# Performance work log

Measured on AMD Instinct MI355X. Metric: run time of the kernel, lower is better.

Reference implementation:

```python
import jax, jax.numpy as jnp
import numpy as np
from jax import lax

VOCAB = 50257; IN_DIM = 1024; MEM = 1024
ATT_UNITS = 256; HOPS = 16
H1 = 1024; H2 = 512; H3 = 256; CLASSES = 5
N = 512  # maxlen == number of tree nodes (pad() is a no-op, penalty mask is zero)


def _build_tree(n):
    # Binary heap tree relabeled to DFS post-order ranks, so children always
    # have smaller rank than their parent and H accumulates in the same order
    # as the original recursive torch code.
    order = []
    def post(j):
        for c in (2 * j + 1, 2 * j + 2):
            if c < n:
                post(c)
        order.append(j)
    post(0)
    rank = {j: r for r, j in enumerate(order)}
    child_idx = np.zeros((n, 2), np.int32)
    mask = np.zeros((n, 2), np.float32)
    for j in range(n):
        r = rank[j]
        for k, c in enumerate((2 * j + 1, 2 * j + 2)):
            if c < n:
                child_idx[r, k] = rank[c]
                mask[r, k] = 1.0
    return jnp.asarray(child_idx), jnp.asarray(mask)


def setup_inputs() -> dict:
    key = jax.random.key(0)
    ks = jax.random.split(key, 24)
    def w(k, shape, s=0.05):
        return jax.random.normal(k, shape, jnp.float32) * s
    child_idx, child_mask = _build_tree(N)
    return {
        "linputs": jax.random.randint(ks[0], (N,), 0, VOCAB, jnp.int32),
        "rinputs": jax.random.randint(ks[1], (N,), 0, VOCAB, jnp.int32),
        "child_idx": child_idx,
        "child_mask": child_mask,
        "emb": w(ks[2], (VOCAB, IN_DIM)),
        "w_ioux": w(ks[3], (3 * MEM, IN_DIM)), "b_ioux": w(ks[4], (3 * MEM,)),
        "w_iouh": w(ks[5], (3 * MEM, MEM)), "b_iouh": w(ks[6], (3 * MEM,)),
        "w_fx": w(ks[7], (MEM, IN_DIM)), "b_fx": w(ks[8], (MEM,)),
        "w_fh": w(ks[9], (MEM, MEM)), "b_fh": w(ks[10], (MEM,)),
        "ws1": w(ks[11], (ATT_UNITS, MEM)),
        "ws2": w(ks[12], (HOPS, ATT_UNITS)),
        "wf": w(ks[13], (1, MEM, H1)),
        "w_lat": w(ks[14], (1, HOPS)), "b_lat": w(ks[15], (1,)),
        "w_fc": w(ks[16], (H2, 3 * H1)), "b_fc": w(ks[17], (H2,)),
        "w_out": w(ks[18], (H3, H2)), "b_out": w(ks[19], (H3,)),
        "w_out1": w(ks[20], (CLASSES, H3)), "b_out1": w(ks[21], (CLASSES,)),
    }


def _tree_lstm(x, child_idx, child_mask, w_ioux, b_ioux, w_iouh, b_iouh,
               w_fx, b_fx, w_fh, b_fh):
    # x: [N, in_dim]; nodes in post-order (children before parent).
    # Leaf case of the original (single all-zero child) is reproduced exactly
    # by masked (zero) child rows: child_h_sum = 0 and sum(f * child_c) = 0.
    n = x.shape[0]
    mem = w_fh.shape[0]
    x_iou = x @ w_ioux.T + b_ioux  # [N, 3M], precomputed input projections
    x_f = x @ w_fx.T + b_fx        # [N, M]

    def step(carry, xs):
        C, Hs = carry
        i, ci, m, xiou, xf = xs
        ch = Hs[ci] * m[:, None]   # [2, M] masked child hidden states
        cc = C[ci] * m[:, None]    # [2, M] masked child cell states
        iou = xiou + ch.sum(0) @ w_iouh.T + b_iouh
        ig, og, ug = jnp.split(iou, 3)
        ig = jax.nn.sigmoid(ig); og = jax.nn.sigmoid(og); ug = jnp.tanh(ug)
        f = jax.nn.sigmoid(ch @ w_fh.T + b_fh + xf)  # [2, M] forget per child
        c = ig * ug + (f * cc).sum(0)
        h = og * jnp.tanh(c)
        return (C.at[i].set(c), Hs.at[i].set(h)), None

    z = jnp.zeros((n, mem), x.dtype)
    (C, Hs), _ = lax.scan(step, (z, z),
                          (jnp.arange(n), child_idx, child_mask, x_iou, x_f))
    return Hs  # H stacked in DFS post-order; root hidden is Hs[-1]


def _attend(H, ws1, ws2):
    # H: [N, M]; N == maxlen so the penalty term of the original is all-zero.
    hbar = jnp.tanh(H @ ws1.T)                           # [N, att_units]
    alphas = jax.nn.softmax((hbar @ ws2.T).T, axis=-1)   # [hops, N]
    return alphas @ H, alphas[None]                      # [hops, M], [1, hops, N]


def reference(linputs, rinputs, child_idx, child_mask, emb,
              w_ioux, b_ioux, w_iouh, b_iouh, w_fx, b_fx, w_fh, b_fh,
              ws1, ws2, wf, w_lat, b_lat, w_fc, b_fc, w_out, b_out,
              w_out1, b_out1):
    tl = lambda tok: _tree_lstm(emb[tok], child_idx, child_mask,
                                w_ioux, b_ioux, w_iouh, b_iouh,
                                w_fx, b_fx, w_fh, b_fh)
    Hl = tl(linputs)
    Hr = tl(rinputs)
    Ml, attl = _attend(Hl, ws1, ws2)
    Mr, attr = _attend(Hr, ws1, ws2)
    lstate = jax.nn.relu(Ml @ wf[0])   # [hops, H1]
    rstate = jax.nn.relu(Mr @ wf[0])
    # lat_att applied on transposed matrix == left-multiply by its weight row
    lvec = w_lat @ lstate + b_lat      # [1, H1]
    rvec = w_lat @ rstate + b_lat
    fr = jnp.concatenate([jnp.abs(lvec - rvec), lvec * rvec,
                          0.5 * (lvec + rvec)], axis=1)  # [1, 3*H1]
    fc = jax.nn.leaky_relu(fr @ w_fc.T + b_fc, 0.01)
    fc2 = jax.nn.sigmoid(fc @ w_out.T + b_out)
    out = jax.nn.log_softmax(fc2 @ w_out1.T + b_out1, axis=-1)  # [1, classes]
    return out, attl, attr
```

## Files before the change

### kernel.cpp

```cpp
#include <hip/hip_runtime.h>
#include <math.h>

#define NN 512
#define MEMD 1024
#define NBLK 256

typedef __attribute__((ext_vector_type(8))) short short8;
typedef __attribute__((ext_vector_type(4))) float float4v;

struct Sched {
  int child0[NN]; int child1[NN];
  float m0[NN]; float m1[NN];
  int chrow[2 * NN];
  int order[NN];
  int lvl_off[12];
};

constexpr void post_order_rec(int j, int n, int (&ord)[NN], int& cnt) {
  if (2 * j + 1 < n) post_order_rec(2 * j + 1, n, ord, cnt);
  if (2 * j + 2 < n) post_order_rec(2 * j + 2, n, ord, cnt);
  ord[cnt++] = j;
}

constexpr Sched make_sched() {
  Sched s{};
  int ord[NN] = {}; int cnt = 0;
  post_order_rec(0, NN, ord, cnt);
  int rank[NN] = {};
  for (int r = 0; r < NN; ++r) rank[ord[r]] = r;
  for (int j = 0; j < NN; ++j) {
    int r = rank[j];
    int c0 = 2 * j + 1, c1 = 2 * j + 2;
    s.child0[r] = (c0 < NN) ? rank[c0] : 0;
    s.m0[r] = (c0 < NN) ? 1.0f : 0.0f;
    s.child1[r] = (c1 < NN) ? rank[c1] : 0;
    s.m1[r] = (c1 < NN) ? 1.0f : 0.0f;
  }
  int h[NN] = {};
  for (int r = 0; r < NN; ++r) {
    int hh = 0;
    if (s.m0[r] > 0.0f) { int t = h[s.child0[r]] + 1; if (t > hh) hh = t; }
    if (s.m1[r] > 0.0f) { int t = h[s.child1[r]] + 1; if (t > hh) hh = t; }
    h[r] = hh;
  }
  int counts[12] = {};
  for (int r = 0; r < NN; ++r) counts[h[r]]++;
  s.lvl_off[0] = 0;
  for (int l = 0; l < 11; ++l) s.lvl_off[l + 1] = s.lvl_off[l] + counts[l];
  int pos[12] = {};
  for (int l = 0; l < 12; ++l) pos[l] = s.lvl_off[l];
  for (int r = 0; r < NN; ++r) s.order[pos[h[r]]++] = r;
  for (int slot = 0; slot < NN; ++slot) {
    int r = s.order[slot];
    s.chrow[2 * slot + 0] = (s.m0[r] > 0.f) ? s.child0[r] : -1;
    s.chrow[2 * slot + 1] = (s.m1[r] > 0.f) ? s.child1[r] : -1;
  }
  return s;
}

static constexpr Sched g_sched = make_sched();
__constant__ Sched c_sched = g_sched;

__device__ __forceinline__ float sigm(float x) { return 1.0f / (1.0f + expf(-x)); }

__device__ __forceinline__ unsigned short f2bf(float f) {
  union { float f; unsigned int u; } v; v.f = f;
  unsigned int r = v.u + 0x7fffu + ((v.u >> 16) & 1u);
  return (unsigned short)(r >> 16);
}

__device__ __forceinline__ void glds16(const unsigned short* g, unsigned short* l) {
  __builtin_amdgcn_global_load_lds(
      (const __attribute__((address_space(1))) void*)g,
      (__attribute__((address_space(3))) void*)l, 16, 0, 0);
}

struct KArgs {
  const int* lin; const int* rin;
  const float* emb;
  const float* w_ioux; const float* b_ioux;
  const float* w_iouh; const float* b_iouh;
  const float* w_fx; const float* b_fx;
  const float* w_fh; const float* b_fh;
  const float* ws1; const float* ws2; const float* wf;
  const float* w_lat; const float* b_lat;
  const float* w_fc; const float* b_fc;
  const float* w_out; const float* b_out;
  const float* w_out1; const float* b_out1;
  float* out;
  float* XO; float* H; float* C; float* HBR; float* LG; float* M; float* TMP;
  float* FR; float* FC;
  unsigned short* Ae; unsigned short* Wxp; unsigned short* Whp;
  unsigned short* Hb; unsigned short* Ws1b;
  unsigned int* sc; unsigned int* sg;
};

__device__ __forceinline__ void gsync(unsigned int* sc, unsigned int* sg) {
  __syncthreads();
  if (threadIdx.x == 0) {
    unsigned int g = __hip_atomic_load(sg, __ATOMIC_RELAXED, __HIP_MEMORY_SCOPE_AGENT);
    unsigned int a = __hip_atomic_fetch_add(sc, 1u, __ATOMIC_ACQ_REL, __HIP_MEMORY_SCOPE_AGENT);
    if (a == (unsigned int)(NBLK - 1)) {
      __hip_atomic_store(sc, 0u, __ATOMIC_RELAXED, __HIP_MEMORY_SCOPE_AGENT);
      __hip_atomic_store(sg, g + 1u, __ATOMIC_RELEASE, __HIP_MEMORY_SCOPE_AGENT);
    } else {
      while (__hip_atomic_load(sg, __ATOMIC_RELAXED, __HIP_MEMORY_SCOPE_AGENT) == g)
        __builtin_amdgcn_s_sleep(1);
      (void)__hip_atomic_load(sg, __ATOMIC_ACQUIRE, __HIP_MEMORY_SCOPE_AGENT);
    }
  }
  __syncthreads();
}

__device__ float* gemm_tile(
    const unsigned short* __restrict__ A, const unsigned short* __restrict__ B,
    int off, int R, int k0, int nt, int bx, int by, char* smem)
{
  unsigned short* As = (unsigned short*)smem;
  unsigned short* Bs = (unsigned short*)(smem + 32768);
  const int tid = threadIdx.x;
  const int L = tid & 63, w = tid >> 6;
  const int q = (L & 7) ^ (L >> 3);

  const unsigned short* ga[4];
  const unsigned short* gb[4];
  #pragma unroll
  for (int i = 0; i < 4; ++i) {
    int c = w * 4 + i;
    int r = 8 * c + (L >> 3);
    int u = bx * 128 + r;
    int arow;
    if (off < 0) {
      arow = u;
    } else {
      if (u >= 4 * R) arow = 1024;
      else {
        int t = (u >= 2 * R) ? 1 : 0;
        int rr = u - t * 2 * R;
        int ch = c_sched.chrow[2 * (off + (rr >> 1)) + (rr & 1)];
        arow = (ch < 0) ? 1024 : t * 512 + ch;
      }
    }
    ga[i] = A + (size_t)arow * 1024 + k0 + q * 8;
    gb[i] = B + (size_t)(by * 128 + r) * 1024 + k0 + q * 8;
  }

  float4v acc[4][4];
  #pragma unroll
  for (int i = 0; i < 4; ++i)
    #pragma unroll
    for (int j = 0; j < 4; ++j) acc[i][j] = (float4v)(0.0f);

  const int wm = (w & 1) * 64, wn = (w >> 1) * 64;
  const int lr = L & 15, lq = L >> 4;

  #pragma unroll
  for (int i = 0; i < 4; ++i) {
    glds16(ga[i], As + (w * 4 + i) * 512);
    glds16(gb[i], Bs + (w * 4 + i) * 512);
    ga[i] += 64; gb[i] += 64;
  }
  __syncthreads();

  int cur = 0;
  for (int kk = 0; kk < nt; ++kk) {
    if (kk + 1 < nt) {
      #pragma unroll
      for (int i = 0; i < 4; ++i) {
        glds16(ga[i], As + (cur ^ 1) * 8192 + (w * 4 + i) * 512);
        glds16(gb[i], Bs + (cur ^ 1) * 8192 + (w * 4 + i) * 512);
        ga[i] += 64; gb[i] += 64;
      }
    }
    const unsigned short* Ac = As + cur * 8192;
    const unsigned short* Bc = Bs + cur * 8192;
    #pragma unroll
    for (int kh = 0; kh < 2; ++kh) {
      short8 af[4], bf[4];
      #pragma unroll
      for (int mi = 0; mi < 4; ++mi) {
        int tr = wm + mi * 16 + lr;
        af[mi] = *(const short8*)(Ac + tr * 64 + (((kh * 4 + lq) ^ (tr & 7)) * 8));
      }
      #pragma unroll
      for (int ni = 0; ni < 4; ++ni) {
        int tr = wn + ni * 16 + lr;
        bf[ni] = *(const short8*)(Bc + tr * 64 + (((kh * 4 + lq) ^ (tr & 7)) * 8));
      }
      #pragma unroll
      for (int mi = 0; mi < 4; ++mi)
        #pragma unroll
        for (int ni = 0; ni < 4; ++ni)
          acc[mi][ni] = __builtin_amdgcn_mfma_f32_16x16x32_bf16(
              af[mi], bf[ni], acc[mi][ni], 0, 0, 0);
    }
    __syncthreads();
    cur ^= 1;
  }

  float* T = (float*)smem;
  #pragma unroll
  for (int mi = 0; mi < 4; ++mi)
    #pragma unroll
    for (int reg = 0; reg < 4; ++reg) {
      int tr = wm + mi * 16 + lq * 4 + reg;
      #pragma unroll
      for (int ni = 0; ni < 4; ++ni)
        T[tr * 128 + wn + ni * 16 + lr] = acc[mi][ni][reg];
    }
  __syncthreads();
  return T;
}

__global__ __launch_bounds__(256) void k_mega(KArgs a)
{
  __shared__ __align__(16) char smem[65536];
  const int bid = (int)blockIdx.x;
  const int tid = (int)threadIdx.x;

  {
    const int t4 = tid * 4;
    for (int u = bid; u < 9473; u += NBLK) {
      if (u < 9472) {
        const float* src; unsigned short* dst;
        if (u < 4096) {
          int r = u & 127, g = r >> 5;
          int c = (u >> 7) * 32 + (r & 31);
          src = (g < 3) ? a.w_ioux + (size_t)(g * 1024 + c) * 1024
                        : a.w_fx + (size_t)c * 1024;
          dst = a.Wxp + (size_t)u * 1024;
        } else if (u < 8192) {
          int p = u - 4096;
          int r = p & 127, g = r >> 5;
          int c = (p >> 7) * 32 + (r & 31);
          src = (g < 3) ? a.w_iouh + (size_t)(g * 1024 + c) * 1024
                        : a.w_fh + (size_t)c * 1024;
          dst = a.Whp + (size_t)p * 1024;
        } else if (u < 8448) {
          int p = u - 8192;
          src = a.ws1 + (size_t)p * 1024;
          dst = a.Ws1b + (size_t)p * 1024;
        } else {
          int p = u - 8448;
          int tok = (p < 512) ? a.lin[p] : a.rin[p - 512];
          src = a.emb + (size_t)tok * 1024;
          dst = a.Ae + (size_t)p * 1024;
        }
        float4 v = *(const float4*)(src + t4);
        ushort4 o;
        o.x = f2bf(v.x); o.y = f2bf(v.y); o.z = f2bf(v.z); o.w = f2bf(v.w);
        *(ushort4*)(dst + t4) = o;
      } else {
        ushort4 z; z.x = 0; z.y = 0; z.z = 0; z.w = 0;
        *(ushort4*)(a.Hb + (size_t)1024 * 1024 + t4) = z;
      }
    }
  }
  gsync(a.sc, a.sg);

  {
    int bx = bid >> 5, by = bid & 31;
    float* T = gemm_tile(a.Ae, a.Wxp, -1, 0, 0, 16, bx, by, smem);
    for (int e = tid; e < 128 * 128; e += 256) {
      int rr = e >> 7, cc = e & 127, g = cc >> 5;
      a.XO[(size_t)(bx * 128 + rr) * 4096 + g * 1024 + by * 32 + (cc & 31)] =
          T[rr * 128 + cc];
    }
    for (int e = tid; e < 128 * 32; e += 256) {
      int rr = e >> 5, ccl = e & 31;
      int row = bx * 128 + rr;
      int rank = row & 511;
      if (c_sched.m0[rank] == 0.0f) {
        int d = by * 32 + ccl;
        float gi = T[rr * 128 + ccl]      + a.b_ioux[d]        + a.b_iouh[d];
        float go = T[rr * 128 + 32 + ccl] + a.b_ioux[1024 + d] + a.b_iouh[1024 + d];
        float gu = T[rr * 128 + 64 + ccl] + a.b_ioux[2048 + d] + a.b_iouh[2048 + d];
        float cv = sigm(gi) * tanhf(gu);
        float hv = sigm(go) * tanhf(cv);
        a.C[(size_t)row * MEMD + d] = cv;
        a.H[(size_t)row * MEMD + d] = hv;
        a.Hb[(size_t)row * MEMD + d] = f2bf(hv);
      }
    }
  }
  gsync(a.sc, a.sg);

  for (int l = 1; l <= 9; ++l) {
    int off = c_sched.lvl_off[l];
    int R = c_sched.lvl_off[l + 1] - off;
    int gx = (4 * R + 127) >> 7;
    int nb = gx << 5;
    if (bid < nb) {
      int bx = bid >> 5, by = bid & 31;
      float* T = gemm_tile(a.Hb, a.Whp, off, R, 0, 16, bx, by, smem);
      int rows = 4 * R - bx * 128; if (rows > 128) rows = 128;
      int pairs = rows >> 1;
      for (int e = tid; e < pairs * 32; e += 256) {
        int p = e >> 5, ccl = e & 31;
        int u0 = bx * 128 + 2 * p;
        int tt = (u0 >= 2 * R) ? 1 : 0;
        int rr = u0 - tt * 2 * R;
        int slot = off + (rr >> 1);
        int node = c_sched.order[slot];
        int d = by * 32 + ccl;
        size_t row = (size_t)tt * 512 + node;
        const float* T0 = T + (2 * p) * 128;
        const float* T1 = T + (2 * p + 1) * 128;
        float gi = a.XO[row * 4096 + d]        + T0[ccl]      + T1[ccl]
                 + a.b_ioux[d] + a.b_iouh[d];
        float go = a.XO[row * 4096 + 1024 + d] + T0[32 + ccl] + T1[32 + ccl]
                 + a.b_ioux[1024 + d] + a.b_iouh[1024 + d];
        float gu = a.XO[row * 4096 + 2048 + d] + T0[64 + ccl] + T1[64 + ccl]
                 + a.b_ioux[2048 + d] + a.b_iouh[2048 + d];
        float xf = a.XO[row * 4096 + 3072 + d] + a.b_fx[d] + a.b_fh[d];
        float f0 = sigm(T0[96 + ccl] + xf);
        float f1 = sigm(T1[96 + ccl] + xf);
        int c0 = c_sched.child0[node], c1 = c_sched.child1[node];
        float cc0 = c_sched.m0[node] * a.C[((size_t)tt * 512 + c0) * MEMD + d];
        float cc1 = c_sched.m1[node] * a.C[((size_t)tt * 512 + c1) * MEMD + d];
        float cv = sigm(gi) * tanhf(gu) + f0 * cc0 + f1 * cc1;
        float hv = sigm(go) * tanhf(cv);
        a.C[row * MEMD + d] = cv;
        a.H[row * MEMD + d] = hv;
        a.Hb[row * MEMD + d] = f2bf(hv);
      }
    }
    gsync(a.sc, a.sg);
  }

  if (bid < 64) {
    int z = bid & 3, by = (bid >> 2) & 1, bx = bid >> 3;
    float* T = gemm_tile(a.Hb, a.Ws1b, -1, 0, z * 256, 4, bx, by, smem);
    for (int e = tid; e < 128 * 128; e += 256) {
      int rr = e >> 7, cc = e & 127;
      a.HBR[(size_t)z * 262144 + (size_t)(bx * 128 + rr) * 256 + by * 128 + cc] =
          T[rr * 128 + cc];
    }
  }
  gsync(a.sc, a.sg);

  if (bid < 8) {
    float* hb = (float*)smem;
    float* w2 = (float*)(smem + 128 * 65 * 4);
    const int t = bid >> 2;
    const int n0 = (bid & 3) * 128;
    for (int e = tid; e < 16 * 256; e += 256) w2[e] = a.ws2[e];
    const int n = tid & 127;
    const int hbase = (tid >> 7) * 8;
    float acc2[8] = {};
    for (int a0 = 0; a0 < 256; a0 += 64) {
      __syncthreads();
      for (int e = tid; e < 128 * 64; e += 256) {
        int rr = e >> 6, aa = e & 63;
        size_t idx = (size_t)(t * 512 + n0 + rr) * 256 + a0 + aa;
        float v = a.HBR[idx] + a.HBR[262144 + idx] + a.HBR[2 * 262144 + idx]
                + a.HBR[3 * 262144 + idx];
        hb[rr * 65 + aa] = tanhf(v);
      }
      __syncthreads();
      for (int aa = 0; aa < 64; ++aa) {
        float v = hb[n * 65 + aa];
        #pragma unroll
        for (int hh = 0; hh < 8; ++hh) acc2[hh] += v * w2[(hbase + hh) * 256 + a0 + aa];
      }
    }
    #pragma unroll
    for (int hh = 0; hh < 8; ++hh)
      a.LG[(size_t)(t * 16 + hbase + hh) * 512 + n0 + n] = acc2[hh];
  }
  gsync(a.sc, a.sg);

  if (bid < 8) {
    float* al = (float*)smem;
    const int t = bid >> 2;
    const int m0 = (bid & 3) * 256;
    for (int e = tid; e < 8192; e += 256) al[e] = a.LG[(size_t)t * 8192 + e];
    __syncthreads();
    const int h = tid >> 4, i = tid & 15;
    float mx = -1e30f;
    #pragma unroll
    for (int j = 0; j < 32; ++j) mx = fmaxf(mx, al[h * 512 + i + 16 * j]);
    #pragma unroll
    for (int m2 = 8; m2 >= 1; m2 >>= 1) mx = fmaxf(mx, __shfl_xor(mx, m2, 64));
    float ev[32]; float s = 0.f;
    #pragma unroll
    for (int j = 0; j < 32; ++j) { ev[j] = expf(al[h * 512 + i + 16 * j] - mx); s += ev[j]; }
    #pragma unroll
    for (int m2 = 8; m2 >= 1; m2 >>= 1) s += __shfl_xor(s, m2, 64);
    float inv = 1.0f / s;
    #pragma unroll
    for (int j = 0; j < 32; ++j) al[h * 512 + i + 16 * j] = ev[j] * inv;
    __syncthreads();
    if ((bid & 3) == 0) {
      for (int e = tid; e < 8192; e += 256)
        a.out[5 + (size_t)t * 8192 + e] = al[e];
    }
    float acc3[16] = {};
    for (int n = 0; n < 512; ++n) {
      float hv = a.H[((size_t)t * 512 + n) * MEMD + m0 + tid];
      #pragma unroll
      for (int hh = 0; hh < 16; ++hh) acc3[hh] += al[hh * 512 + n] * hv;
    }
    #pragma unroll
    for (int hh = 0; hh < 16; ++hh)
      a.M[((size_t)t * 16 + hh) * MEMD + m0 + tid] = acc3[hh];
  }
  gsync(a.sc, a.sg);

  if (bid < 32) {
    float* Ms = (float*)smem;
    const int t = bid / 16;
    const int rem = bid % 16;
    const int h0 = (rem / 4) * 4;
    const int o0 = (rem % 4) * 256;
    for (int e = tid; e < 4 * 1024; e += 256)
      Ms[e] = a.M[((size_t)t * 16 + h0 + (e >> 10)) * MEMD + (e & 1023)];
    __syncthreads();
    float acc4[4] = {};
    for (int m = 0; m < 1024; ++m) {
      float wv = a.wf[(size_t)m * 1024 + o0 + tid];
      #pragma unroll
      for (int h = 0; h < 4; ++h) acc4[h] += Ms[h * 1024 + m] * wv;
    }
    #pragma unroll
    for (int h = 0; h < 4; ++h)
      a.TMP[((size_t)t * 16 + h0 + h) * 1024 + o0 + tid] = acc4[h];
  }
  gsync(a.sc, a.sg);

  if (bid < 4) {
    const int o = bid * 256 + tid;
    const float blat = a.b_lat[0];
    float lv = blat, rv = blat;
    #pragma unroll
    for (int h = 0; h < 16; ++h) {
      float wlh = a.w_lat[h];
      lv += wlh * fmaxf(a.TMP[(size_t)h * 1024 + o], 0.0f);
      rv += wlh * fmaxf(a.TMP[(size_t)(16 + h) * 1024 + o], 0.0f);
    }
    a.FR[o] = fabsf(lv - rv);
    a.FR[1024 + o] = lv * rv;
    a.FR[2048 + o] = 0.5f * (lv + rv);
  }
  gsync(a.sc, a.sg);

  {
    float* red = (float*)smem;
    for (int rep = 0; rep < 2; ++rep) {
      int j = bid + rep * 256;
      const float* wrow = a.w_fc + (size_t)j * 3072;
      float acc5 = 0.f;
      #pragma unroll
      for (int i2 = 0; i2 < 12; ++i2) {
        int k = tid + i2 * 256;
        acc5 += a.FR[k] * wrow[k];
      }
      red[tid] = acc5;
      __syncthreads();
      for (int s2 = 128; s2 > 0; s2 >>= 1) {
        if (tid < s2) red[tid] += red[tid + s2];
        __syncthreads();
      }
      if (tid == 0) {
        float v = red[0] + a.b_fc[j];
        a.FC[j] = (v > 0.f) ? v : 0.01f * v;
      }
      __syncthreads();
    }
  }
  gsync(a.sc, a.sg);

  if (bid == 0) {
    float* sh = (float*)smem;
    float* lg5 = sh + 256;
    const float* wrow = a.w_out + (size_t)tid * 512;
    float acc6 = 0.f;
    #pragma unroll 8
    for (int k = 0; k < 512; ++k) acc6 += a.FC[k] * wrow[k];
    sh[tid] = 1.0f / (1.0f + expf(-(acc6 + a.b_out[tid])));
    __syncthreads();
    if (tid < 160) {
      const int cls = tid >> 5, lane = tid & 31;
      float v = 0.f;
      #pragma unroll
      for (int j = 0; j < 8; ++j) {
        int k = lane + 32 * j;
        v += sh[k] * a.w_out1[(size_t)cls * 256 + k];
      }
      #pragma unroll
      for (int m2 = 16; m2 >= 1; m2 >>= 1) v += __shfl_xor(v, m2, 64);
      if (lane == 0) lg5[cls] = v + a.b_out1[cls];
    }
    __syncthreads();
    if (tid == 0) {
      float mx = lg5[0];
      for (int k = 1; k < 5; ++k) mx = fmaxf(mx, lg5[k]);
      float s2 = 0.f;
      for (int k = 0; k < 5; ++k) s2 += expf(lg5[k] - mx);
      float lse = mx + logf(s2);
      for (int k = 0; k < 5; ++k) a.out[k] = lg5[k] - lse;
    }
  }
}

extern "C" void kernel_launch(void* const* d_in, const int* in_sizes, int n_in,
                              void* d_out, int out_size, void* d_ws, size_t ws_size,
                              hipStream_t stream)
{
  KArgs ka;
  ka.lin    = (const int*)d_in[0];
  ka.rin    = (const int*)d_in[1];
  ka.emb    = (const float*)d_in[4];
  ka.w_ioux = (const float*)d_in[5];
  ka.b_ioux = (const float*)d_in[6];
  ka.w_iouh = (const float*)d_in[7];
  ka.b_iouh = (const float*)d_in[8];
  ka.w_fx   = (const float*)d_in[9];
  ka.b_fx   = (const float*)d_in[10];
  ka.w_fh   = (const float*)d_in[11];
  ka.b_fh   = (const float*)d_in[12];
  ka.ws1    = (const float*)d_in[13];
  ka.ws2    = (const float*)d_in[14];
  ka.wf     = (const float*)d_in[15];
  ka.w_lat  = (const float*)d_in[16];
  ka.b_lat  = (const float*)d_in[17];
  ka.w_fc   = (const float*)d_in[18];
  ka.b_fc   = (const float*)d_in[19];
  ka.w_out  = (const float*)d_in[20];
  ka.b_out  = (const float*)d_in[21];
  ka.w_out1 = (const float*)d_in[22];
  ka.b_out1 = (const float*)d_in[23];
  ka.out    = (float*)d_out;

  float* fws = (float*)d_ws;
  ka.XO  = fws;
  ka.H   = ka.XO  + 1024 * 4096;
  ka.C   = ka.H   + 1024 * 1024;
  ka.HBR = ka.C   + 1024 * 1024;
  ka.LG  = ka.HBR + 4 * 1024 * 256;
  ka.M   = ka.LG  + 16384;
  ka.TMP = ka.M   + 32768;
  ka.FR  = ka.TMP + 32768;
  ka.FC  = ka.FR  + 3072;
  ka.Ae   = (unsigned short*)(ka.FC + 512);
  ka.Wxp  = ka.Ae  + 1024 * 1024;
  ka.Whp  = ka.Wxp + 4096 * 1024;
  ka.Hb   = ka.Whp + 4096 * 1024;
  ka.Ws1b = ka.Hb  + 1025 * 1024;
  ka.sc   = (unsigned int*)(ka.Ws1b + 256 * 1024);
  ka.sg   = ka.sc + 64;

  hipMemsetAsync((void*)ka.sc, 0, 512, stream);
  void* params[1] = { (void*)&ka };
  hipLaunchCooperativeKernel((const void*)k_mega, dim3(NBLK), dim3(256),
                             params, 0, stream);
}
```

Measured before the change: 877.3 us.

## Replace full-grid barriers with monotonic done-counter and per-phase participant waits

Swaps the all-block generation barrier for a single monotonic completion counter that only the blocks active in a phase increment, via hierarchical per-group sub-counters. Each later phase waits until the counter reaches a precomputed cumulative threshold, so idle blocks no longer join every barrier and can exit early. The fc stage is also moved onto 64 blocks doing 8 rows each, which cuts the number of participants in that phase. In exchange the hardcoded thresholds must exactly match the phase participant counts, and more counter memory has to be zeroed.

```diff
diff --git a/kernel.cpp b/kernel.cpp
--- a/kernel.cpp
+++ b/kernel.cpp
@@ -92,24 +92,33 @@
   float* FR; float* FC;
   unsigned short* Ae; unsigned short* Wxp; unsigned short* Whp;
   unsigned short* Hb; unsigned short* Ws1b;
-  unsigned int* sc; unsigned int* sg;
+  unsigned int* sc;
 };
 
-__device__ __forceinline__ void gsync(unsigned int* sc, unsigned int* sg) {
+__device__ __forceinline__ void wait_done(unsigned int* done, unsigned int T) {
+  if (threadIdx.x == 0) {
+    while (__hip_atomic_load(done, __ATOMIC_RELAXED, __HIP_MEMORY_SCOPE_AGENT) < T)
+      __builtin_amdgcn_s_sleep(4);
+    (void)__hip_atomic_load(done, __ATOMIC_ACQUIRE, __HIP_MEMORY_SCOPE_AGENT);
+  }
+  __syncthreads();
+}
+
+__device__ __forceinline__ void arrive(unsigned int* sc, int p, int nb) {
   __syncthreads();
   if (threadIdx.x == 0) {
-    unsigned int g = __hip_atomic_load(sg, __ATOMIC_RELAXED, __HIP_MEMORY_SCOPE_AGENT);
-    unsigned int a = __hip_atomic_fetch_add(sc, 1u, __ATOMIC_ACQ_REL, __HIP_MEMORY_SCOPE_AGENT);
-    if (a == (unsigned int)(NBLK - 1)) {
-      __hip_atomic_store(sc, 0u, __ATOMIC_RELAXED, __HIP_MEMORY_SCOPE_AGENT);
-      __hip_atomic_store(sg, g + 1u, __ATOMIC_RELEASE, __HIP_MEMORY_SCOPE_AGENT);
-    } else {
-      while (__hip_atomic_load(sg, __ATOMIC_RELAXED, __HIP_MEMORY_SCOPE_AGENT) == g)
-        __builtin_amdgcn_s_sleep(1);
-      (void)__hip_atomic_load(sg, __ATOMIC_ACQUIRE, __HIP_MEMORY_SCOPE_AGENT);
-    }
-  }
-  __syncthreads();
+    int b = (int)blockIdx.x;
+    int g = b >> 5;
+    int gsz = nb - (g << 5); if (gsz > 32) gsz = 32;
+    unsigned int* gc = sc + 16 + (size_t)(p * 8 + g) * 16;
+    unsigned int a = __hip_atomic_fetch_add(gc, 1u, __ATOMIC_RELEASE,
+                                            __HIP_MEMORY_SCOPE_AGENT);
+    if (a == (unsigned int)(gsz - 1)) {
+      __threadfence();
+      __hip_atomic_fetch_add(sc, (unsigned int)gsz, __ATOMIC_RELEASE,
+                             __HIP_MEMORY_SCOPE_AGENT);
+    }
+  }
 }
 
 __device__ float* gemm_tile(
@@ -217,6 +226,7 @@
   __shared__ __align__(16) char smem[65536];
   const int bid = (int)blockIdx.x;
   const int tid = (int)threadIdx.x;
+  unsigned int* done = a.sc;
 
   {
     const int t4 = tid * 4;
@@ -256,9 +266,10 @@
       }
     }
   }
-  gsync(a.sc, a.sg);
+  arrive(a.sc, 0, 256);
 
   {
+    wait_done(done, 256);
     int bx = bid >> 5, by = bid & 31;
     float* T = gemm_tile(a.Ae, a.Wxp, -1, 0, 0, 16, bx, by, smem);
     for (int e = tid; e < 128 * 128; e += 256) {
@@ -283,52 +294,58 @@
       }
     }
   }
-  gsync(a.sc, a.sg);
-
-  for (int l = 1; l <= 9; ++l) {
-    int off = c_sched.lvl_off[l];
-    int R = c_sched.lvl_off[l + 1] - off;
-    int gx = (4 * R + 127) >> 7;
-    int nb = gx << 5;
-    if (bid < nb) {
-      int bx = bid >> 5, by = bid & 31;
-      float* T = gemm_tile(a.Hb, a.Whp, off, R, 0, 16, bx, by, smem);
-      int rows = 4 * R - bx * 128; if (rows > 128) rows = 128;
-      int pairs = rows >> 1;
-      for (int e = tid; e < pairs * 32; e += 256) {
-        int p = e >> 5, ccl = e & 31;
-        int u0 = bx * 128 + 2 * p;
-        int tt = (u0 >= 2 * R) ? 1 : 0;
-        int rr = u0 - tt * 2 * R;
-        int slot = off + (rr >> 1);
-        int node = c_sched.order[slot];
-        int d = by * 32 + ccl;
-        size_t row = (size_t)tt * 512 + node;
-        const float* T0 = T + (2 * p) * 128;
-        const float* T1 = T + (2 * p + 1) * 128;
-        float gi = a.XO[row * 4096 + d]        + T0[ccl]      + T1[ccl]
-                 + a.b_ioux[d] + a.b_iouh[d];
-        float go = a.XO[row * 4096 + 1024 + d] + T0[32 + ccl] + T1[32 + ccl]
-                 + a.b_ioux[1024 + d] + a.b_iouh[1024 + d];
-        float gu = a.XO[row * 4096 + 2048 + d] + T0[64 + ccl] + T1[64 + ccl]
-                 + a.b_ioux[2048 + d] + a.b_iouh[2048 + d];
-        float xf = a.XO[row * 4096 + 3072 + d] + a.b_fx[d] + a.b_fh[d];
-        float f0 = sigm(T0[96 + ccl] + xf);
-        float f1 = sigm(T1[96 + ccl] + xf);
-        int c0 = c_sched.child0[node], c1 = c_sched.child1[node];
-        float cc0 = c_sched.m0[node] * a.C[((size_t)tt * 512 + c0) * MEMD + d];
-        float cc1 = c_sched.m1[node] * a.C[((size_t)tt * 512 + c1) * MEMD + d];
-        float cv = sigm(gi) * tanhf(gu) + f0 * cc0 + f1 * cc1;
-        float hv = sigm(go) * tanhf(cv);
-        a.C[row * MEMD + d] = cv;
-        a.H[row * MEMD + d] = hv;
-        a.Hb[row * MEMD + d] = f2bf(hv);
-      }
-    }
-    gsync(a.sc, a.sg);
+  arrive(a.sc, 1, 256);
+
+  {
+    const unsigned int lvlT[10] =
+        {0, 512, 640, 704, 736, 768, 800, 832, 864, 896};
+    for (int l = 1; l <= 9; ++l) {
+      int off = c_sched.lvl_off[l];
+      int R = c_sched.lvl_off[l + 1] - off;
+      int gx = (4 * R + 127) >> 7;
+      int nb = gx << 5;
+      if (bid < nb) {
+        wait_done(done, lvlT[l]);
+        int bx = bid >> 5, by = bid & 31;
+        float* T = gemm_tile(a.Hb, a.Whp, off, R, 0, 16, bx, by, smem);
+        int rows = 4 * R - bx * 128; if (rows > 128) rows = 128;
+        int pairs = rows >> 1;
+        for (int e = tid; e < pairs * 32; e += 256) {
+          int p = e >> 5, ccl = e & 31;
+          int u0 = bx * 128 + 2 * p;
+          int tt = (u0 >= 2 * R) ? 1 : 0;
+          int rr = u0 - tt * 2 * R;
+          int slot = off + (rr >> 1);
+          int node = c_sched.order[slot];
+          int d = by * 32 + ccl;
+          size_t row = (size_t)tt * 512 + node;
+          const float* T0 = T + (2 * p) * 128;
+          const float* T1 = T + (2 * p + 1) * 128;
+          float gi = a.XO[row * 4096 + d]        + T0[ccl]      + T1[ccl]
+                   + a.b_ioux[d] + a.b_iouh[d];
+          float go = a.XO[row * 4096 + 1024 + d] + T0[32 + ccl] + T1[32 + ccl]
+                   + a.b_ioux[1024 + d] + a.b_iouh[1024 + d];
+          float gu = a.XO[row * 4096 + 2048 + d] + T0[64 + ccl] + T1[64 + ccl]
+                   + a.b_ioux[2048 + d] + a.b_iouh[2048 + d];
+          float xf = a.XO[row * 4096 + 3072 + d] + a.b_fx[d] + a.b_fh[d];
+          float f0 = sigm(T0[96 + ccl] + xf);
+          float f1 = sigm(T1[96 + ccl] + xf);
+          int c0 = c_sched.child0[node], c1 = c_sched.child1[node];
+          float cc0 = c_sched.m0[node] * a.C[((size_t)tt * 512 + c0) * MEMD + d];
+          float cc1 = c_sched.m1[node] * a.C[((size_t)tt * 512 + c1) * MEMD + d];
+          float cv = sigm(gi) * tanhf(gu) + f0 * cc0 + f1 * cc1;
+          float hv = sigm(go) * tanhf(cv);
+          a.C[row * MEMD + d] = cv;
+          a.H[row * MEMD + d] = hv;
+          a.Hb[row * MEMD + d] = f2bf(hv);
+        }
+        arrive(a.sc, 1 + l, nb);
+      }
+    }
   }
 
   if (bid < 64) {
+    wait_done(done, 928);
     int z = bid & 3, by = (bid >> 2) & 1, bx = bid >> 3;
     float* T = gemm_tile(a.Hb, a.Ws1b, -1, 0, z * 256, 4, bx, by, smem);
     for (int e = tid; e < 128 * 128; e += 256) {
@@ -336,10 +353,11 @@
       a.HBR[(size_t)z * 262144 + (size_t)(bx * 128 + rr) * 256 + by * 128 + cc] =
           T[rr * 128 + cc];
     }
-  }
-  gsync(a.sc, a.sg);
+    arrive(a.sc, 11, 64);
+  }
 
   if (bid < 8) {
+    wait_done(done, 992);
     float* hb = (float*)smem;
     float* w2 = (float*)(smem + 128 * 65 * 4);
     const int t = bid >> 2;
@@ -367,10 +385,11 @@
     #pragma unroll
     for (int hh = 0; hh < 8; ++hh)
       a.LG[(size_t)(t * 16 + hbase + hh) * 512 + n0 + n] = acc2[hh];
-  }
-  gsync(a.sc, a.sg);
+    arrive(a.sc, 12, 8);
+  }
 
   if (bid < 8) {
+    wait_done(done, 1000);
     float* al = (float*)smem;
     const int t = bid >> 2;
     const int m0 = (bid & 3) * 256;
@@ -404,10 +423,11 @@
     #pragma unroll
     for (int hh = 0; hh < 16; ++hh)
       a.M[((size_t)t * 16 + hh) * MEMD + m0 + tid] = acc3[hh];
-  }
-  gsync(a.sc, a.sg);
+    arrive(a.sc, 13, 8);
+  }
 
   if (bid < 32) {
+    wait_done(done, 1008);
     float* Ms = (float*)smem;
     const int t = bid / 16;
     const int rem = bid % 16;
@@ -425,10 +445,11 @@
     #pragma unroll
     for (int h = 0; h < 4; ++h)
       a.TMP[((size_t)t * 16 + h0 + h) * 1024 + o0 + tid] = acc4[h];
-  }
-  gsync(a.sc, a.sg);
+    arrive(a.sc, 14, 32);
+  }
 
   if (bid < 4) {
+    wait_done(done, 1040);
     const int o = bid * 256 + tid;
     const float blat = a.b_lat[0];
     float lv = blat, rv = blat;
@@ -441,13 +462,14 @@
     a.FR[o] = fabsf(lv - rv);
     a.FR[1024 + o] = lv * rv;
     a.FR[2048 + o] = 0.5f * (lv + rv);
-  }
-  gsync(a.sc, a.sg);
-
-  {
+    arrive(a.sc, 15, 4);
+  }
+
+  if (bid < 64) {
+    wait_done(done, 1044);
     float* red = (float*)smem;
-    for (int rep = 0; rep < 2; ++rep) {
-      int j = bid + rep * 256;
+    for (int rep = 0; rep < 8; ++rep) {
+      int j = bid * 8 + rep;
       const float* wrow = a.w_fc + (size_t)j * 3072;
       float acc5 = 0.f;
       #pragma unroll
@@ -467,10 +489,11 @@
       }
       __syncthreads();
     }
-  }
-  gsync(a.sc, a.sg);
+    arrive(a.sc, 16, 64);
+  }
 
   if (bid == 0) {
+    wait_done(done, 1108);
     float* sh = (float*)smem;
     float* lg5 = sh + 256;
     const float* wrow = a.w_out + (size_t)tid * 512;
@@ -548,9 +571,8 @@
   ka.Hb   = ka.Whp + 4096 * 1024;
   ka.Ws1b = ka.Hb  + 1025 * 1024;
   ka.sc   = (unsigned int*)(ka.Ws1b + 256 * 1024);
-  ka.sg   = ka.sc + 64;
-
-  hipMemsetAsync((void*)ka.sc, 0, 512, stream);
+
+  hipMemsetAsync((void*)ka.sc, 0, 9216, stream);
   void* params[1] = { (void*)&ka };
   hipLaunchCooperativeKernel((const void*)k_mega, dim3(NBLK), dim3(256),
                              params, 0, stream);
```

Result: faster. 818.5 us (-6.7%).
